# Kernel optimization log

Hardware: AMD Instinct MI355X
Metric: run time of the kernel (lower is better)

## Reference

```python
import jax, jax.numpy as jnp
import numpy as np

N = 50000      # nodes
E = 640000     # edges
D = 128        # input_dim
H = 128        # hidden_channels
L = 2          # n_layers
NG = 512       # number of graphs
NC = 1         # n_classes
BN_EPS = 1e-5


def _bn(x, gamma, beta):
    # BatchNorm1d over node dim, batch statistics (biased var), eps=1e-5
    mu = jnp.mean(x, axis=0)
    var = jnp.mean((x - mu) ** 2, axis=0)
    return (x - mu) * jax.lax.rsqrt(var + BN_EPS) * gamma + beta


def setup_inputs() -> dict:
    key = jax.random.key(0)
    ks = jax.random.split(key, 16)
    s = 0.05
    x = jax.random.normal(ks[0], (N, D), dtype=jnp.float32)
    edge_index = jax.random.randint(ks[1], (2, E), 0, N, dtype=jnp.int64)
    batch = jnp.sort(jax.random.randint(ks[2], (N,), 0, NG, dtype=jnp.int64))
    return {
        "x": x,
        "edge_index": edge_index,
        "batch": batch,
        "lin_in_w": jax.random.normal(ks[3], (D, H), dtype=jnp.float32) * s,
        "lin_in_b": jnp.zeros((H,), dtype=jnp.float32),
        "mlp_w1": jax.random.normal(ks[4], (L, H, H), dtype=jnp.float32) * s,
        "mlp_b1": jnp.zeros((L, H), dtype=jnp.float32),
        "bn1_g": jnp.ones((L, H), dtype=jnp.float32),
        "bn1_b": jnp.zeros((L, H), dtype=jnp.float32),
        "mlp_w2": jax.random.normal(ks[5], (L, H, H), dtype=jnp.float32) * s,
        "mlp_b2": jnp.zeros((L, H), dtype=jnp.float32),
        "bn_g": jnp.ones((L, H), dtype=jnp.float32),
        "bn_b": jnp.zeros((L, H), dtype=jnp.float32),
        "jk_w": jax.random.normal(ks[6], (L * H, NC), dtype=jnp.float32) * s,
        "jk_b": jnp.zeros((NC,), dtype=jnp.float32),
    }


def reference(x, edge_index, batch, lin_in_w, lin_in_b, mlp_w1, mlp_b1,
              bn1_g, bn1_b, mlp_w2, mlp_b2, bn_g, bn_b, jk_w, jk_b):
    src, dst = edge_index[0], edge_index[1]
    n = x.shape[0]
    h = x @ lin_in_w + lin_in_b  # [N, H]
    outs = []
    for l in range(mlp_w1.shape[0]):
        # GINConv (eps=0): mlp(x + sum_{j in N(i)} x_j)
        agg = jax.ops.segment_sum(h[src], dst, num_segments=n)
        z = h + agg
        z = z @ mlp_w1[l] + mlp_b1[l]
        z = jax.nn.relu(_bn(z, bn1_g[l], bn1_b[l]))
        z = z @ mlp_w2[l] + mlp_b2[l]
        # outer BatchNorm + ReLU; dropout is identity in eval
        h = jax.nn.relu(_bn(z, bn_g[l], bn_b[l]))
        outs.append(h)
    hcat = jnp.concatenate(outs, axis=-1)  # [N, L*H]
    # global mean pool per graph
    counts = jax.ops.segment_sum(jnp.ones((n,), dtype=hcat.dtype), batch, num_segments=NG)
    pooled = jax.ops.segment_sum(hcat, batch, num_segments=NG)
    pooled = pooled / jnp.maximum(counts, 1.0)[:, None]
    return pooled @ jk_w + jk_b  # [NG, n_classes]
```

## Files before the change

### kernel.cpp

```cpp
#include <hip/hip_runtime.h>
#include <cstddef>

#define NN 50000
#define NE 640000
#define NG 512
#define NL 2
#define NSLOT 16
constexpr float BN_EPS = 1e-5f;

typedef __attribute__((ext_vector_type(8))) short bf16x8;
typedef __attribute__((ext_vector_type(16))) float f32x16;

__device__ inline float b2f_lo(unsigned int u) {
  union { unsigned int i; float f; } v; v.i = u << 16; return v.f;
}
__device__ inline float b2f_hi(unsigned int u) {
  union { unsigned int i; float f; } v; v.i = u & 0xffff0000u; return v.f;
}
__device__ inline unsigned short f2b(float f) {
  union { float f; unsigned int i; } v; v.f = f;
  return (unsigned short)((v.i + 0x7fffu + ((v.i >> 16) & 1u)) >> 16);
}
__device__ inline unsigned int pack2(float lo, float hi) {
  return (unsigned int)f2b(lo) | ((unsigned int)f2b(hi) << 16);
}
__device__ inline int swz(int row, int b) { return row * 256 + (b ^ ((row & 15) << 4)); }

__device__ inline void unpack_add(const uint4 v, float* a) {
  a[0] += b2f_lo(v.x); a[1] += b2f_hi(v.x); a[2] += b2f_lo(v.y); a[3] += b2f_hi(v.y);
  a[4] += b2f_lo(v.z); a[5] += b2f_hi(v.z); a[6] += b2f_lo(v.w); a[7] += b2f_hi(v.w);
}

__device__ inline void bn_from_stats(const float* __restrict__ st,
                                     const float* __restrict__ gamma,
                                     const float* __restrict__ beta, int c,
                                     float& sc, float& sh) {
  float s = 0.f, s2 = 0.f;
  #pragma unroll
  for (int b = 0; b < NSLOT; ++b) {
    s += st[b * 128 + c];
    s2 += st[2048 + b * 128 + c];
  }
  const float inv_n = 1.f / (float)NN;
  const float mu = s * inv_n;
  const float var = fmaxf(s2 * inv_n - mu * mu, 0.f);
  sc = rsqrtf(var + BN_EPS) * gamma[c];
  sh = beta[c] - mu * sc;
}

__global__ __launch_bounds__(256) void gemm_gather32(
    const unsigned short* __restrict__ h, const int* __restrict__ rowptr,
    const int* __restrict__ pck, const unsigned short* __restrict__ Wt,
    const float* __restrict__ bias, unsigned short* __restrict__ C,
    float* __restrict__ psum, float* __restrict__ psq, int n) {
  __shared__ uint4 Au[16][32];
  __shared__ float colsum[128];
  __shared__ float colsq[128];
  const int t = threadIdx.x;
  const int row0 = blockIdx.x * 32;

  if (t < 128) { colsum[t] = 0.f; colsq[t] = 0.f; }

  const int ln = t & 31;
  const int cg = t >> 5;
  const int gr = row0 + ln;
  const uint4* h4 = (const uint4*)h;
  float a0[8], a1[8];
  #pragma unroll
  for (int p = 0; p < 8; ++p) { a0[p] = 0.f; a1[p] = 0.f; }
  if (gr < n) {
    {
      const uint4* p = &h4[(size_t)gr * 16 + cg * 2];
      unpack_add(p[0], a0); unpack_add(p[1], a1);
    }
    const int beg = rowptr[gr], end = rowptr[gr + 1];
    int j = beg;
    for (; j + 1 < end; j += 2) {
      const int s0i = pck[j] & 0x01FFFFFF;
      const int s1i = pck[j + 1] & 0x01FFFFFF;
      const uint4* p0 = &h4[(size_t)s0i * 16 + cg * 2];
      const uint4* p1 = &h4[(size_t)s1i * 16 + cg * 2];
      const uint4 v00 = p0[0], v01 = p0[1];
      const uint4 v10 = p1[0], v11 = p1[1];
      unpack_add(v00, a0); unpack_add(v01, a1);
      unpack_add(v10, a0); unpack_add(v11, a1);
    }
    if (j < end) {
      const int s0i = pck[j] & 0x01FFFFFF;
      const uint4* p0 = &h4[(size_t)s0i * 16 + cg * 2];
      unpack_add(p0[0], a0); unpack_add(p0[1], a1);
    }
  }
  {
    uint4 o0, o1;
    o0.x = pack2(a0[0], a0[1]); o0.y = pack2(a0[2], a0[3]);
    o0.z = pack2(a0[4], a0[5]); o0.w = pack2(a0[6], a0[7]);
    o1.x = pack2(a1[0], a1[1]); o1.y = pack2(a1[2], a1[3]);
    o1.z = pack2(a1[4], a1[5]); o1.w = pack2(a1[6], a1[7]);
    Au[cg * 2][ln] = o0;
    Au[cg * 2 + 1][ln] = o1;
  }
  __syncthreads();

  const int w = t >> 6;
  const int l = t & 63;
  const int lane31 = l & 31;
  const int khalf = l >> 5;

  f32x16 acc;
  #pragma unroll
  for (int i = 0; i < 16; ++i) acc[i] = 0.f;

  const unsigned short* Bp = Wt + (size_t)(w * 32 + lane31) * 128 + 8 * khalf;
  #pragma unroll
  for (int k0 = 0; k0 < 8; ++k0) {
    const bf16x8 aF = *(const bf16x8*)&Au[k0 * 2 + khalf][lane31];
    const bf16x8 bF = *(const bf16x8*)(Bp + k0 * 16);
    acc = __builtin_amdgcn_mfma_f32_32x32x16_bf16(aF, bF, acc, 0, 0, 0);
  }

  const int col = w * 32 + lane31;
  const float bs = bias[col];
  float s0 = 0.f, q0 = 0.f;
  #pragma unroll
  for (int r = 0; r < 16; ++r) {
    const int row = (r & 3) + 8 * (r >> 2) + 4 * khalf;
    const int grow = row0 + row;
    if (grow < n) {
      const float v = acc[r] + bs;
      C[(size_t)grow * 128 + col] = f2b(v);
      s0 += v; q0 = fmaf(v, v, q0);
    }
  }
  atomicAdd(&colsum[col], s0);
  atomicAdd(&colsq[col], q0);
  __syncthreads();
  if (t < 128) {
    const int slot = blockIdx.x & (NSLOT - 1);
    atomicAdd(&psum[slot * 128 + t], colsum[t]);
    atomicAdd(&psq[slot * 128 + t], colsq[t]);
  }
}

template <int MODE, bool STATS>
__global__ __launch_bounds__(256) void gemm_fused(
    const void* __restrict__ Ain, const float* __restrict__ stIn,
    const float* __restrict__ gIn, const float* __restrict__ beIn,
    const unsigned short* __restrict__ Wt, const float* __restrict__ bias,
    unsigned short* __restrict__ C, float* __restrict__ psum,
    float* __restrict__ psq, int n) {
  __shared__ char Al[16384];
  __shared__ float colsum[128];
  __shared__ float colsq[128];
  __shared__ float sc_s[128], sh_s[128];
  const int t = threadIdx.x;
  const int row0 = blockIdx.x * 64;

  if (t < 128) {
    if (STATS) { colsum[t] = 0.f; colsq[t] = 0.f; }
    if (MODE == 2) {
      float a, b;
      bn_from_stats(stIn, gIn, beIn, t, a, b);
      sc_s[t] = a; sh_s[t] = b;
    }
  }
  if (MODE == 2) __syncthreads();

  #pragma unroll
  for (int ii = 0; ii < 4; ++ii) {
    const int i = t + ii * 256;
    const int r = i >> 4;
    const int u = (i & 15) << 4;
    const int gr = row0 + r;
    uint4 v = make_uint4(0u, 0u, 0u, 0u);
    if (gr < n) {
      if (MODE == 3) {
        const float* Af = (const float*)Ain;
        const float4 f0 = *(const float4*)(Af + (size_t)gr * 128 + (u >> 1));
        const float4 f1 = *(const float4*)(Af + (size_t)gr * 128 + (u >> 1) + 4);
        v.x = pack2(f0.x, f0.y); v.y = pack2(f0.z, f0.w);
        v.z = pack2(f1.x, f1.y); v.w = pack2(f1.z, f1.w);
      } else {
        v = *(const uint4*)((const char*)Ain + (size_t)gr * 256 + u);
        const int c0 = u >> 1;
        unsigned int pw[4] = {v.x, v.y, v.z, v.w};
        #pragma unroll
        for (int p = 0; p < 4; ++p) {
          float lo = b2f_lo(pw[p]);
          float hi = b2f_hi(pw[p]);
          lo = fmaxf(fmaf(lo, sc_s[c0 + 2 * p], sh_s[c0 + 2 * p]), 0.f);
          hi = fmaxf(fmaf(hi, sc_s[c0 + 2 * p + 1], sh_s[c0 + 2 * p + 1]), 0.f);
          pw[p] = pack2(lo, hi);
        }
        v = make_uint4(pw[0], pw[1], pw[2], pw[3]);
      }
    }
    *(uint4*)(Al + swz(r, u)) = v;
  }
  __syncthreads();

  const int w = t >> 6;
  const int l = t & 63;
  const int lane31 = l & 31;
  const int khalf = l >> 5;
  const int mrow = (w & 1) * 32;
  const int c0 = (w >> 1) * 64;

  f32x16 acc0, acc1;
  #pragma unroll
  for (int i = 0; i < 16; ++i) { acc0[i] = 0.f; acc1[i] = 0.f; }

  const unsigned short* Bp0 = Wt + (size_t)(c0 + lane31) * 128 + 8 * khalf;
  const unsigned short* Bp1 = Wt + (size_t)(c0 + 32 + lane31) * 128 + 8 * khalf;

  #pragma unroll
  for (int k0 = 0; k0 < 128; k0 += 16) {
    const int kb = (k0 + 8 * khalf) * 2;
    const bf16x8 a  = *(const bf16x8*)(Al + swz(mrow + lane31, kb));
    const bf16x8 b0 = *(const bf16x8*)(Bp0 + k0);
    const bf16x8 b1 = *(const bf16x8*)(Bp1 + k0);
    acc0 = __builtin_amdgcn_mfma_f32_32x32x16_bf16(a, b0, acc0, 0, 0, 0);
    acc1 = __builtin_amdgcn_mfma_f32_32x32x16_bf16(a, b1, acc1, 0, 0, 0);
  }

  const float bias0 = bias[c0 + lane31];
  const float bias1 = bias[c0 + 32 + lane31];
  float s0 = 0.f, q0 = 0.f, s1 = 0.f, q1 = 0.f;
  #pragma unroll
  for (int r = 0; r < 16; ++r) {
    const int row = mrow + (r & 3) + 8 * (r >> 2) + 4 * khalf;
    const int grow = row0 + row;
    if (grow < n) {
      const float v0 = acc0[r] + bias0;
      const float v1 = acc1[r] + bias1;
      C[(size_t)grow * 128 + c0 + lane31] = f2b(v0);
      C[(size_t)grow * 128 + c0 + 32 + lane31] = f2b(v1);
      if (STATS) {
        s0 += v0; q0 = fmaf(v0, v0, q0);
        s1 += v1; q1 = fmaf(v1, v1, q1);
      }
    }
  }
  if (STATS) {
    atomicAdd(&colsum[c0 + lane31], s0);
    atomicAdd(&colsq[c0 + lane31], q0);
    atomicAdd(&colsum[c0 + 32 + lane31], s1);
    atomicAdd(&colsq[c0 + 32 + lane31], q1);
    __syncthreads();
    if (t < 128) {
      const int slot = blockIdx.x & (NSLOT - 1);
      atomicAdd(&psum[slot * 128 + t], colsum[t]);
      atomicAdd(&psq[slot * 128 + t], colsq[t]);
    }
  }
}

__global__ __launch_bounds__(256) void setup_k(
    const float* __restrict__ lw, const float* __restrict__ w1,
    const float* __restrict__ w2, unsigned short* __restrict__ Wt,
    const int* __restrict__ batch, int* __restrict__ gstart,
    float* __restrict__ counts, int* __restrict__ cnt,
    float* __restrict__ stats) {
  const int b = blockIdx.x, t = threadIdx.x;
  if (b < 320) {
    const int i = b * 256 + t;
    const int m = i >> 14, r = i & 16383;
    const int ncol = r >> 7, k = r & 127;
    const float* src = (m == 0) ? lw : (m <= 2) ? (w1 + (m - 1) * 16384)
                                                : (w2 + (m - 3) * 16384);
    Wt[i] = f2b(src[k * 128 + ncol]);
  } else if (b < 516) {
    const int i = (b - 320) * 256 + t;
    if (i < NN) cnt[i] = 0;
  } else if (b < 580) {
    stats[(b - 516) * 256 + t] = 0.f;
  } else {
    const int g = (b - 580) * 256 + t;
    if (g > NG) return;
    int lo = 0, hi = NN;
    while (lo < hi) { int m = (lo + hi) >> 1; if (batch[m] < g) lo = m + 1; else hi = m; }
    gstart[g] = lo;
    if (g < NG) {
      int lo1 = lo, hi1 = NN;
      while (lo1 < hi1) { int m = (lo1 + hi1) >> 1; if (batch[m] < g + 1) lo1 = m + 1; else hi1 = m; }
      counts[g] = (float)(lo1 - lo);
    }
  }
}

#define SCAN_B 196
__global__ __launch_bounds__(256) void edge_hist(const int* __restrict__ ei,
                                                 int* __restrict__ cnt) {
  const int e = blockIdx.x * 256 + threadIdx.x;
  if (e >= NE) return;
  atomicAdd(&cnt[ei[NE + e]], 1);
}

__global__ __launch_bounds__(256) void scan1(const int* __restrict__ cnt,
                                             int* __restrict__ rowptr,
                                             int* __restrict__ bsum) {
  __shared__ int s[256];
  const int b = blockIdx.x, t = threadIdx.x;
  const int i = b * 256 + t;
  const int v = (i < NN) ? cnt[i] : 0;
  s[t] = v;
  __syncthreads();
  for (int off = 1; off < 256; off <<= 1) {
    const int x = (t >= off) ? s[t - off] : 0;
    __syncthreads();
    s[t] += x;
    __syncthreads();
  }
  if (i < NN) rowptr[i] = s[t] - v;
  if (t == 255) bsum[b] = s[255];
}

__global__ __launch_bounds__(256) void scan2(const int* __restrict__ bsum,
                                             int* __restrict__ boff,
                                             int* __restrict__ rowptrN) {
  __shared__ int s[256];
  const int t = threadIdx.x;
  const int v = (t < SCAN_B) ? bsum[t] : 0;
  s[t] = v;
  __syncthreads();
  for (int off = 1; off < 256; off <<= 1) {
    const int x = (t >= off) ? s[t - off] : 0;
    __syncthreads();
    s[t] += x;
    __syncthreads();
  }
  if (t < SCAN_B) boff[t] = s[t] - v;
  if (t == 255) *rowptrN = s[255];
}

__global__ __launch_bounds__(256) void scan3(int* __restrict__ rowptr,
                                             const int* __restrict__ boff,
                                             int* __restrict__ cursor) {
  const int i = blockIdx.x * 256 + threadIdx.x;
  if (i < NN) {
    const int v = rowptr[i] + boff[blockIdx.x];
    rowptr[i] = v;
    cursor[i] = v;
  }
}

__global__ __launch_bounds__(256) void build_csr(const int* __restrict__ ei,
                                                 int* __restrict__ cursor,
                                                 int* __restrict__ pck) {
  const int e = blockIdx.x * 256 + threadIdx.x;
  if (e >= NE) return;
  const int src = ei[e];
  const int dst = ei[NE + e];
  const int pos = atomicAdd(&cursor[dst], 1);
  pck[pos] = src | ((dst & 31) << 25);
}

template <bool WRITE_H, bool FINAL>
__global__ __launch_bounds__(256) void bn_relu_pool_seg_b(
    const unsigned short* __restrict__ Z, const float* __restrict__ stIn,
    const float* __restrict__ gIn, const float* __restrict__ beIn,
    const int* __restrict__ gstart, unsigned short* __restrict__ h,
    float* __restrict__ pooled, int layerOff,
    const float* __restrict__ counts, const float* __restrict__ jkw,
    const float* __restrict__ jkb, float* __restrict__ out) {
  __shared__ float sc_s[128], sh_s[128];
  __shared__ float red[256 * 8];
  const int g = blockIdx.x;
  const int t = threadIdx.x;
  if (t < 128) {
    float a, b;
    bn_from_stats(stIn, gIn, beIn, t, a, b);
    sc_s[t] = a; sh_s[t] = b;
  }
  __syncthreads();
  const int r0 = gstart[g], r1 = gstart[g + 1];
  const int q = t & 15;
  const int rr = t >> 4;
  const int c0 = q * 8;
  float sc[8], sh[8], acc[8];
  #pragma unroll
  for (int i = 0; i < 8; ++i) { sc[i] = sc_s[c0 + i]; sh[i] = sh_s[c0 + i]; acc[i] = 0.f; }
  for (int r = r0 + rr; r < r1; r += 16) {
    const uint4 v = ((const uint4*)Z)[(size_t)r * 16 + q];
    float o[8];
    o[0] = b2f_lo(v.x); o[1] = b2f_hi(v.x); o[2] = b2f_lo(v.y); o[3] = b2f_hi(v.y);
    o[4] = b2f_lo(v.z); o[5] = b2f_hi(v.z); o[6] = b2f_lo(v.w); o[7] = b2f_hi(v.w);
    #pragma unroll
    for (int i = 0; i < 8; ++i) {
      o[i] = fmaxf(fmaf(o[i], sc[i], sh[i]), 0.f);
      acc[i] += o[i];
    }
    if (WRITE_H) {
      uint4 ov;
      ov.x = pack2(o[0], o[1]); ov.y = pack2(o[2], o[3]);
      ov.z = pack2(o[4], o[5]); ov.w = pack2(o[6], o[7]);
      ((uint4*)h)[(size_t)r * 16 + q] = ov;
    }
  }
  #pragma unroll
  for (int i = 0; i < 8; ++i) red[t * 8 + i] = acc[i];
  __syncthreads();
  for (int off = 8; off >= 1; off >>= 1) {
    if (rr < off) {
      #pragma unroll
      for (int i = 0; i < 8; ++i)
        red[t * 8 + i] += red[(t + off * 16) * 8 + i];
    }
    __syncthreads();
  }
  if (!FINAL) {
    if (rr == 0) {
      #pragma unroll
      for (int i = 0; i < 8; ++i)
        pooled[(size_t)g * 256 + layerOff + c0 + i] = red[t * 8 + i];
    }
  } else {
    float part = 0.f;
    if (t < 128)
      part = pooled[(size_t)g * 256 + t] * jkw[t] + red[t] * jkw[128 + t];
    red[1024 + t] = part;
    __syncthreads();
    for (int off = 64; off >= 1; off >>= 1) {
      if (t < off) red[1024 + t] += red[1024 + t + off];
      __syncthreads();
    }
    if (t == 0)
      out[g] = red[1024] / fmaxf(counts[g], 1.f) + jkb[0];
  }
}

extern "C" void kernel_launch(void* const* d_in, const int* in_sizes, int n_in,
                              void* d_out, int out_size, void* d_ws,
                              size_t ws_size, hipStream_t stream) {
  const float* x     = (const float*)d_in[0];
  const int*   ei    = (const int*)d_in[1];
  const int*   batch = (const int*)d_in[2];
  const float* lin_w = (const float*)d_in[3];
  const float* lin_b = (const float*)d_in[4];
  const float* w1    = (const float*)d_in[5];
  const float* b1    = (const float*)d_in[6];
  const float* g1    = (const float*)d_in[7];
  const float* be1   = (const float*)d_in[8];
  const float* w2    = (const float*)d_in[9];
  const float* b2    = (const float*)d_in[10];
  const float* g2    = (const float*)d_in[11];
  const float* be2   = (const float*)d_in[12];
  const float* jkw   = (const float*)d_in[13];
  const float* jkb   = (const float*)d_in[14];
  float* out = (float*)d_out;

  char* base = (char*)d_ws;
  unsigned short* hb  = (unsigned short*)base;
  unsigned short* agb = hb + (size_t)NN * 128;
  unsigned short* WtA = agb + (size_t)NN * 128;
  float* pooled = (float*)(WtA + 5 * 16384);
  float* counts = pooled + (size_t)NG * 256;
  int* gstart = (int*)(counts + NG);
  int* rowptr = gstart + NG + 4;
  int* bsum   = rowptr + NN + 4;
  int* boff   = bsum + 200;
  int* pck    = boff + 200;
  int* cnt    = pck + NE;
  float* stats = (float*)(cnt + NN);

  setup_k<<<583, 256, 0, stream>>>(lin_w, w1, w2, WtA, batch, gstart, counts,
                                   cnt, stats);

  edge_hist<<<(NE + 255) / 256, 256, 0, stream>>>(ei, cnt);
  scan1<<<SCAN_B, 256, 0, stream>>>(cnt, rowptr, bsum);
  scan2<<<1, 256, 0, stream>>>(bsum, boff, rowptr + NN);
  scan3<<<SCAN_B, 256, 0, stream>>>(rowptr, boff, cnt);
  build_csr<<<(NE + 255) / 256, 256, 0, stream>>>(ei, cnt, pck);

  const int gemm_grid = (NN + 63) / 64;
  const int gath_grid = (NN + 31) / 32;

  float* st1_0 = stats;
  float* st2_0 = stats + 4096;
  float* st1_1 = stats + 2 * 4096;
  float* st2_1 = stats + 3 * 4096;

  gemm_fused<3, false><<<gemm_grid, 256, 0, stream>>>(
      x, nullptr, nullptr, nullptr, WtA, lin_b, hb, nullptr, nullptr, NN);

  gemm_gather32<<<gath_grid, 256, 0, stream>>>(
      hb, rowptr, pck, WtA + 1 * 16384, b1, agb, st1_0, st1_0 + 2048, NN);
  gemm_fused<2, true><<<gemm_grid, 256, 0, stream>>>(
      agb, st1_0, g1, be1, WtA + 3 * 16384, b2, agb, st2_0, st2_0 + 2048, NN);
  bn_relu_pool_seg_b<true, false><<<NG, 256, 0, stream>>>(
      agb, st2_0, g2, be2, gstart, hb, pooled, 0,
      nullptr, nullptr, nullptr, nullptr);

  gemm_gather32<<<gath_grid, 256, 0, stream>>>(
      hb, rowptr, pck, WtA + 2 * 16384, b1 + 128, agb, st1_1, st1_1 + 2048, NN);
  gemm_fused<2, true><<<gemm_grid, 256, 0, stream>>>(
      agb, st1_1, g1 + 128, be1 + 128, WtA + 4 * 16384, b2 + 128, agb,
      st2_1, st2_1 + 2048, NN);
  bn_relu_pool_seg_b<false, true><<<NG, 256, 0, stream>>>(
      agb, st2_1, g2 + 128, be2 + 128, gstart, nullptr, pooled, 128,
      counts, jkw, jkb, out);
}
```

Before: 240.2 us.

## Merge input GEMM with CSR build, fuse scan passes, stage GEMM output via LDS

The input projection GEMM and the CSR fill now run as one launch, with the extra blocks handling edge scatter. This lets the two independent jobs share the GPU instead of running back to back. The scan2 and scan3 passes are merged so every block recomputes the block-offset prefix itself, dropping a launch and the boff buffer. GEMM epilogues now write bf16 results into shared memory first and then store full 16-byte rows to global memory, replacing scattered 2-byte stores. The cost is extra barriers and LDS traffic per block.

```diff
diff --git a/kernel.cpp b/kernel.cpp
--- a/kernel.cpp
+++ b/kernel.cpp
@@ -6,6 +6,8 @@
 #define NG 512
 #define NL 2
 #define NSLOT 16
+#define SCAN_B 196
+#define G3_BLKS 782
 constexpr float BN_EPS = 1e-5f;
 
 typedef __attribute__((ext_vector_type(8))) short bf16x8;
@@ -142,9 +144,8 @@
   }
 }
 
-template <int MODE, bool STATS>
-__global__ __launch_bounds__(256) void gemm_fused(
-    const void* __restrict__ Ain, const float* __restrict__ stIn,
+__global__ __launch_bounds__(256) void gemm_bn(
+    const unsigned short* __restrict__ Ain, const float* __restrict__ stIn,
     const float* __restrict__ gIn, const float* __restrict__ beIn,
     const unsigned short* __restrict__ Wt, const float* __restrict__ bias,
     unsigned short* __restrict__ C, float* __restrict__ psum,
@@ -157,14 +158,12 @@
   const int row0 = blockIdx.x * 64;
 
   if (t < 128) {
-    if (STATS) { colsum[t] = 0.f; colsq[t] = 0.f; }
-    if (MODE == 2) {
-      float a, b;
-      bn_from_stats(stIn, gIn, beIn, t, a, b);
-      sc_s[t] = a; sh_s[t] = b;
-    }
-  }
-  if (MODE == 2) __syncthreads();
+    colsum[t] = 0.f; colsq[t] = 0.f;
+    float a, b;
+    bn_from_stats(stIn, gIn, beIn, t, a, b);
+    sc_s[t] = a; sh_s[t] = b;
+  }
+  __syncthreads();
 
   #pragma unroll
   for (int ii = 0; ii < 4; ++ii) {
@@ -174,26 +173,18 @@
     const int gr = row0 + r;
     uint4 v = make_uint4(0u, 0u, 0u, 0u);
     if (gr < n) {
-      if (MODE == 3) {
-        const float* Af = (const float*)Ain;
-        const float4 f0 = *(const float4*)(Af + (size_t)gr * 128 + (u >> 1));
-        const float4 f1 = *(const float4*)(Af + (size_t)gr * 128 + (u >> 1) + 4);
-        v.x = pack2(f0.x, f0.y); v.y = pack2(f0.z, f0.w);
-        v.z = pack2(f1.x, f1.y); v.w = pack2(f1.z, f1.w);
-      } else {
-        v = *(const uint4*)((const char*)Ain + (size_t)gr * 256 + u);
-        const int c0 = u >> 1;
-        unsigned int pw[4] = {v.x, v.y, v.z, v.w};
-        #pragma unroll
-        for (int p = 0; p < 4; ++p) {
-          float lo = b2f_lo(pw[p]);
-          float hi = b2f_hi(pw[p]);
-          lo = fmaxf(fmaf(lo, sc_s[c0 + 2 * p], sh_s[c0 + 2 * p]), 0.f);
-          hi = fmaxf(fmaf(hi, sc_s[c0 + 2 * p + 1], sh_s[c0 + 2 * p + 1]), 0.f);
-          pw[p] = pack2(lo, hi);
-        }
-        v = make_uint4(pw[0], pw[1], pw[2], pw[3]);
+      v = *(const uint4*)((const char*)Ain + (size_t)gr * 256 + u);
+      const int c0 = u >> 1;
+      unsigned int pw[4] = {v.x, v.y, v.z, v.w};
+      #pragma unroll
+      for (int p = 0; p < 4; ++p) {
+        float lo = b2f_lo(pw[p]);
+        float hi = b2f_hi(pw[p]);
+        lo = fmaxf(fmaf(lo, sc_s[c0 + 2 * p], sh_s[c0 + 2 * p]), 0.f);
+        hi = fmaxf(fmaf(hi, sc_s[c0 + 2 * p + 1], sh_s[c0 + 2 * p + 1]), 0.f);
+        pw[p] = pack2(lo, hi);
       }
+      v = make_uint4(pw[0], pw[1], pw[2], pw[3]);
     }
     *(uint4*)(Al + swz(r, u)) = v;
   }
@@ -222,6 +213,7 @@
     acc0 = __builtin_amdgcn_mfma_f32_32x32x16_bf16(a, b0, acc0, 0, 0, 0);
     acc1 = __builtin_amdgcn_mfma_f32_32x32x16_bf16(a, b1, acc1, 0, 0, 0);
   }
+  __syncthreads();
 
   const float bias0 = bias[c0 + lane31];
   const float bias1 = bias[c0 + 32 + lane31];
@@ -229,29 +221,115 @@
   #pragma unroll
   for (int r = 0; r < 16; ++r) {
     const int row = mrow + (r & 3) + 8 * (r >> 2) + 4 * khalf;
-    const int grow = row0 + row;
-    if (grow < n) {
-      const float v0 = acc0[r] + bias0;
-      const float v1 = acc1[r] + bias1;
-      C[(size_t)grow * 128 + c0 + lane31] = f2b(v0);
-      C[(size_t)grow * 128 + c0 + 32 + lane31] = f2b(v1);
-      if (STATS) {
-        s0 += v0; q0 = fmaf(v0, v0, q0);
-        s1 += v1; q1 = fmaf(v1, v1, q1);
-      }
-    }
-  }
-  if (STATS) {
-    atomicAdd(&colsum[c0 + lane31], s0);
-    atomicAdd(&colsq[c0 + lane31], q0);
-    atomicAdd(&colsum[c0 + 32 + lane31], s1);
-    atomicAdd(&colsq[c0 + 32 + lane31], q1);
-    __syncthreads();
-    if (t < 128) {
-      const int slot = blockIdx.x & (NSLOT - 1);
-      atomicAdd(&psum[slot * 128 + t], colsum[t]);
-      atomicAdd(&psq[slot * 128 + t], colsq[t]);
-    }
+    const float v0 = acc0[r] + bias0;
+    const float v1 = acc1[r] + bias1;
+    *(unsigned short*)(Al + swz(row, (c0 + lane31) * 2)) = f2b(v0);
+    *(unsigned short*)(Al + swz(row, (c0 + 32 + lane31) * 2)) = f2b(v1);
+    if (row0 + row < n) {
+      s0 += v0; q0 = fmaf(v0, v0, q0);
+      s1 += v1; q1 = fmaf(v1, v1, q1);
+    }
+  }
+  atomicAdd(&colsum[c0 + lane31], s0);
+  atomicAdd(&colsq[c0 + lane31], q0);
+  atomicAdd(&colsum[c0 + 32 + lane31], s1);
+  atomicAdd(&colsq[c0 + 32 + lane31], q1);
+  __syncthreads();
+
+  #pragma unroll
+  for (int ii = 0; ii < 4; ++ii) {
+    const int i = t + ii * 256;
+    const int r = i >> 4;
+    const int u = (i & 15) << 4;
+    const int gr = row0 + r;
+    if (gr < n)
+      *(uint4*)((char*)C + (size_t)gr * 256 + u) = *(const uint4*)(Al + swz(r, u));
+  }
+  if (t < 128) {
+    const int slot = blockIdx.x & (NSLOT - 1);
+    atomicAdd(&psum[slot * 128 + t], colsum[t]);
+    atomicAdd(&psq[slot * 128 + t], colsq[t]);
+  }
+}
+
+__global__ __launch_bounds__(256) void gemm3_build(
+    const float* __restrict__ x, const unsigned short* __restrict__ Wt,
+    const float* __restrict__ bias, unsigned short* __restrict__ C,
+    const int* __restrict__ ei, int* __restrict__ cursor,
+    int* __restrict__ pck, int n) {
+  __shared__ char Al[16384];
+  const int t = threadIdx.x;
+  if (blockIdx.x >= G3_BLKS) {
+    const int e = (blockIdx.x - G3_BLKS) * 256 + t;
+    if (e < NE) {
+      const int src = ei[e];
+      const int dst = ei[NE + e];
+      const int pos = atomicAdd(&cursor[dst], 1);
+      pck[pos] = src | ((dst & 31) << 25);
+    }
+    return;
+  }
+  const int row0 = blockIdx.x * 64;
+
+  #pragma unroll
+  for (int ii = 0; ii < 4; ++ii) {
+    const int i = t + ii * 256;
+    const int r = i >> 4;
+    const int u = (i & 15) << 4;
+    const int gr = row0 + r;
+    uint4 v = make_uint4(0u, 0u, 0u, 0u);
+    if (gr < n) {
+      const float4 f0 = *(const float4*)(x + (size_t)gr * 128 + (u >> 1));
+      const float4 f1 = *(const float4*)(x + (size_t)gr * 128 + (u >> 1) + 4);
+      v.x = pack2(f0.x, f0.y); v.y = pack2(f0.z, f0.w);
+      v.z = pack2(f1.x, f1.y); v.w = pack2(f1.z, f1.w);
+    }
+    *(uint4*)(Al + swz(r, u)) = v;
+  }
+  __syncthreads();
+
+  const int w = t >> 6;
+  const int l = t & 63;
+  const int lane31 = l & 31;
+  const int khalf = l >> 5;
+  const int mrow = (w & 1) * 32;
+  const int c0 = (w >> 1) * 64;
+
+  f32x16 acc0, acc1;
+  #pragma unroll
+  for (int i = 0; i < 16; ++i) { acc0[i] = 0.f; acc1[i] = 0.f; }
+
+  const unsigned short* Bp0 = Wt + (size_t)(c0 + lane31) * 128 + 8 * khalf;
+  const unsigned short* Bp1 = Wt + (size_t)(c0 + 32 + lane31) * 128 + 8 * khalf;
+
+  #pragma unroll
+  for (int k0 = 0; k0 < 128; k0 += 16) {
+    const int kb = (k0 + 8 * khalf) * 2;
+    const bf16x8 a  = *(const bf16x8*)(Al + swz(mrow + lane31, kb));
+    const bf16x8 b0 = *(const bf16x8*)(Bp0 + k0);
+    const bf16x8 b1 = *(const bf16x8*)(Bp1 + k0);
+    acc0 = __builtin_amdgcn_mfma_f32_32x32x16_bf16(a, b0, acc0, 0, 0, 0);
+    acc1 = __builtin_amdgcn_mfma_f32_32x32x16_bf16(a, b1, acc1, 0, 0, 0);
+  }
+  __syncthreads();
+
+  const float bias0 = bias[c0 + lane31];
+  const float bias1 = bias[c0 + 32 + lane31];
+  #pragma unroll
+  for (int r = 0; r < 16; ++r) {
+    const int row = mrow + (r & 3) + 8 * (r >> 2) + 4 * khalf;
+    *(unsigned short*)(Al + swz(row, (c0 + lane31) * 2)) = f2b(acc0[r] + bias0);
+    *(unsigned short*)(Al + swz(row, (c0 + 32 + lane31) * 2)) = f2b(acc1[r] + bias1);
+  }
+  __syncthreads();
+  #pragma unroll
+  for (int ii = 0; ii < 4; ++ii) {
+    const int i = t + ii * 256;
+    const int r = i >> 4;
+    const int u = (i & 15) << 4;
+    const int gr = row0 + r;
+    if (gr < n)
+      *(uint4*)((char*)C + (size_t)gr * 256 + u) = *(const uint4*)(Al + swz(r, u));
   }
 }
 
@@ -288,7 +366,6 @@
   }
 }
 
-#define SCAN_B 196
 __global__ __launch_bounds__(256) void edge_hist(const int* __restrict__ ei,
                                                  int* __restrict__ cnt) {
   const int e = blockIdx.x * 256 + threadIdx.x;
@@ -315,11 +392,11 @@
   if (t == 255) bsum[b] = s[255];
 }
 
-__global__ __launch_bounds__(256) void scan2(const int* __restrict__ bsum,
-                                             int* __restrict__ boff,
-                                             int* __restrict__ rowptrN) {
+__global__ __launch_bounds__(256) void scan23(int* __restrict__ rowptr,
+                                              const int* __restrict__ bsum,
+                                              int* __restrict__ cursor) {
   __shared__ int s[256];
-  const int t = threadIdx.x;
+  const int blk = blockIdx.x, t = threadIdx.x;
   const int v = (t < SCAN_B) ? bsum[t] : 0;
   s[t] = v;
   __syncthreads();
@@ -329,30 +406,14 @@
     s[t] += x;
     __syncthreads();
   }
-  if (t < SCAN_B) boff[t] = s[t] - v;
-  if (t == 255) *rowptrN = s[255];
-}
-
-__global__ __launch_bounds__(256) void scan3(int* __restrict__ rowptr,
-                                             const int* __restrict__ boff,
-                                             int* __restrict__ cursor) {
-  const int i = blockIdx.x * 256 + threadIdx.x;
+  const int boff = s[blk] - bsum[blk];
+  const int i = blk * 256 + t;
   if (i < NN) {
-    const int v = rowptr[i] + boff[blockIdx.x];
-    rowptr[i] = v;
-    cursor[i] = v;
-  }
-}
-
-__global__ __launch_bounds__(256) void build_csr(const int* __restrict__ ei,
-                                                 int* __restrict__ cursor,
-                                                 int* __restrict__ pck) {
-  const int e = blockIdx.x * 256 + threadIdx.x;
-  if (e >= NE) return;
-  const int src = ei[e];
-  const int dst = ei[NE + e];
-  const int pos = atomicAdd(&cursor[dst], 1);
-  pck[pos] = src | ((dst & 31) << 25);
+    const int r = rowptr[i] + boff;
+    rowptr[i] = r;
+    cursor[i] = r;
+  }
+  if (blk == SCAN_B - 1 && t == 0) rowptr[NN] = s[255];
 }
 
 template <bool WRITE_H, bool FINAL>
@@ -458,8 +519,7 @@
   int* gstart = (int*)(counts + NG);
   int* rowptr = gstart + NG + 4;
   int* bsum   = rowptr + NN + 4;
-  int* boff   = bsum + 200;
-  int* pck    = boff + 200;
+  int* pck    = bsum + 200;
   int* cnt    = pck + NE;
   float* stats = (float*)(cnt + NN);
 
@@ -468,9 +528,10 @@
 
   edge_hist<<<(NE + 255) / 256, 256, 0, stream>>>(ei, cnt);
   scan1<<<SCAN_B, 256, 0, stream>>>(cnt, rowptr, bsum);
-  scan2<<<1, 256, 0, stream>>>(bsum, boff, rowptr + NN);
-  scan3<<<SCAN_B, 256, 0, stream>>>(rowptr, boff, cnt);
-  build_csr<<<(NE + 255) / 256, 256, 0, stream>>>(ei, cnt, pck);
+  scan23<<<SCAN_B, 256, 0, stream>>>(rowptr, bsum, cnt);
+
+  gemm3_build<<<G3_BLKS + (NE + 255) / 256, 256, 0, stream>>>(
+      x, WtA, lin_b, hb, ei, cnt, pck, NN);
 
   const int gemm_grid = (NN + 63) / 64;
   const int gath_grid = (NN + 31) / 32;
@@ -480,12 +541,9 @@
   float* st1_1 = stats + 2 * 4096;
   float* st2_1 = stats + 3 * 4096;
 
-  gemm_fused<3, false><<<gemm_grid, 256, 0, stream>>>(
-      x, nullptr, nullptr, nullptr, WtA, lin_b, hb, nullptr, nullptr, NN);
-
   gemm_gather32<<<gath_grid, 256, 0, stream>>>(
       hb, rowptr, pck, WtA + 1 * 16384, b1, agb, st1_0, st1_0 + 2048, NN);
-  gemm_fused<2, true><<<gemm_grid, 256, 0, stream>>>(
+  gemm_bn<<<gemm_grid, 256, 0, stream>>>(
       agb, st1_0, g1, be1, WtA + 3 * 16384, b2, agb, st2_0, st2_0 + 2048, NN);
   bn_relu_pool_seg_b<true, false><<<NG, 256, 0, stream>>>(
       agb, st2_0, g2, be2, gstart, hb, pooled, 0,
@@ -493,7 +551,7 @@
 
   gemm_gather32<<<gath_grid, 256, 0, stream>>>(
       hb, rowptr, pck, WtA + 2 * 16384, b1 + 128, agb, st1_1, st1_1 + 2048, NN);
-  gemm_fused<2, true><<<gemm_grid, 256, 0, stream>>>(
+  gemm_bn<<<gemm_grid, 256, 0, stream>>>(
       agb, st1_1, g1 + 128, be1 + 128, WtA + 4 * 16384, b2 + 128, agb,
       st2_1, st2_1 + 2048, NN);
   bn_relu_pool_seg_b<false, true><<<NG, 256, 0, stream>>>(
```

After: 238.2 us. Within noise of the previous version (-0.8%).
